# Kernel optimization log

Hardware: AMD Instinct MI355X
Metric: run time of the kernel (lower is better)

## Reference

```python
import jax, jax.numpy as jnp
import numpy as np

D_MODEL = 768
MLP_DIM = 3072
N_EXPERTS = 8
TOP_K = 2
GROUP_DET = 1024
GROUP_CLS = 128


def _route(x, wr, k, capacity):
    """Deterministic top-k softmax router with capacity (vmoe-style).

    x: [G, S, d], wr: [d, E]. Returns dispatch [G,S,E,C] (0/1) and
    combine [G,S,E,C] (gate-weighted).
    """
    G, S, _ = x.shape
    E = wr.shape[1]
    gates = jax.nn.softmax(jnp.einsum('gsd,de->gse', x, wr))  # [G,S,E]
    gval, gidx = jax.lax.top_k(gates, k)                      # [G,S,k]
    # rank-major ordering: all rank-0 choices first, then rank-1, ...
    idx = jnp.swapaxes(gidx, 1, 2).reshape(G, k * S)          # [G,kS]
    val = jnp.swapaxes(gval, 1, 2).reshape(G, k * S)
    oh = jax.nn.one_hot(idx, E, dtype=x.dtype)                # [G,kS,E]
    # position of each assignment in its expert's buffer
    pos = jnp.take_along_axis(jnp.cumsum(oh, axis=1), idx[..., None], axis=2)[..., 0] - 1.0
    keep = (pos < capacity).astype(x.dtype)                   # drop overflow tokens
    posc = jnp.where(pos < capacity, pos, 0.0).astype(jnp.int32)
    slot = jax.nn.one_hot(posc, capacity, dtype=x.dtype)      # [G,kS,C]
    disp = oh[:, :, :, None] * slot[:, :, None, :] * keep[:, :, None, None]  # [G,kS,E,C]
    disp = disp.reshape(G, k, S, E, capacity)
    combine = (disp * val.reshape(G, k, S, 1, 1)).sum(axis=1)  # [G,S,E,C]
    dispatch = disp.sum(axis=1)                                # [G,S,E,C]
    return dispatch, combine


def _expert_mlp(xe, w1, b1, w2, b2):
    # xe: [E,G,C,d]; per-expert params w1:[E,d,m], b1:[E,m], w2:[E,m,d], b2:[E,d]
    h = jax.nn.gelu(jnp.einsum('egcd,edm->egcm', xe, w1) + b1[:, None, None, :])
    return jnp.einsum('egcm,emd->egcd', h, w2) + b2[:, None, None, :]


def _moe_stream(x3, group_size, wr, w1, b1, w2, b2):
    B, S, d = x3.shape
    x = x3.reshape(-1, group_size, d)                         # [G,gs,d]
    capacity = group_size * TOP_K // N_EXPERTS
    dispatch, combine = _route(x, wr, TOP_K, capacity)
    xe = jnp.einsum('gsec,gsd->egcd', dispatch, x)            # gather to experts
    ye = _expert_mlp(xe, w1, b1, w2, b2)                      # grouped MLP
    y = jnp.einsum('gsec,egcd->gsd', combine, ye)             # weighted scatter back
    return y.reshape(B, S, d)


def setup_inputs() -> dict:
    key = jax.random.key(0)
    ks = jax.random.split(key, 8)
    xav1 = float(np.sqrt(6.0 / (D_MODEL + MLP_DIM)))
    xavr = float(np.sqrt(6.0 / (D_MODEL + N_EXPERTS)))
    return {
        'inputs_det': jax.random.normal(ks[0], (8, 1024, D_MODEL), jnp.float32),
        'inputs_cls': jax.random.normal(ks[1], (8, 128, D_MODEL), jnp.float32),
        'wr_det': jax.random.uniform(ks[2], (D_MODEL, N_EXPERTS), jnp.float32, -xavr, xavr),
        'wr_cls': jax.random.uniform(ks[3], (D_MODEL, N_EXPERTS), jnp.float32, -xavr, xavr),
        'w1': jax.random.uniform(ks[4], (N_EXPERTS, D_MODEL, MLP_DIM), jnp.float32, -xav1, xav1),
        'b1': jax.random.normal(ks[5], (N_EXPERTS, MLP_DIM), jnp.float32) * 1e-6,
        'w2': jax.random.uniform(ks[6], (N_EXPERTS, MLP_DIM, D_MODEL), jnp.float32, -xav1, xav1),
        'b2': jax.random.normal(ks[7], (N_EXPERTS, D_MODEL), jnp.float32) * 1e-6,
    }


def reference(inputs_det, inputs_cls, wr_det, wr_cls, w1, b1, w2, b2):
    out_det = _moe_stream(inputs_det, GROUP_DET, wr_det, w1, b1, w2, b2)
    out_cls = _moe_stream(inputs_cls, GROUP_CLS, wr_cls, w1, b1, w2, b2)
    return (out_det, out_cls)
```

## Files before the change

### kernel.cpp

```cpp
#include <hip/hip_runtime.h>
#include <hip/hip_bf16.h>
#include <math.h>

typedef __bf16 bf16;
typedef __bf16 bf16x8 __attribute__((ext_vector_type(8)));
typedef __bf16 bf16x4 __attribute__((ext_vector_type(4)));
typedef float  f32x4  __attribute__((ext_vector_type(4)));

#define D_MODEL 768
#define MLP_DIM 3072

#define SZ_W1T   ((size_t)8*3072*768*2)
#define SZ_W2T   ((size_t)8*768*3072*2)
#define SZ_XED   ((size_t)8*8*256*768*2)
#define SZ_XEC   ((size_t)8*8*32*768*2)
#define SZ_HD    ((size_t)8*2048*3072*2)
#define SZ_HC    ((size_t)8*256*3072*2)
#define SZ_YED   ((size_t)8*2048*768*2)
#define SZ_YEC   ((size_t)8*256*768*2)
#define SZ_RID   ((size_t)8192*8)
#define SZ_RGD   ((size_t)8192*8)
#define SZ_RIC   ((size_t)1024*8)
#define SZ_RGC   ((size_t)1024*8)
#define SZ_STD   ((size_t)8*8*256*4)
#define SZ_STC   ((size_t)8*8*32*4)
#define SZ_TSD   ((size_t)2*8192*4)
#define SZ_TSC   ((size_t)2*1024*4)

#define OFF_W1T  ((size_t)0)
#define OFF_W2T  (OFF_W1T + SZ_W1T)
#define OFF_XED  (OFF_W2T + SZ_W2T)
#define OFF_XEC  (OFF_XED + SZ_XED)
#define OFF_HD   (OFF_XEC + SZ_XEC)
#define OFF_HC   (OFF_HD  + SZ_HD)
#define OFF_YED  (OFF_HC  + SZ_HC)
#define OFF_YEC  (OFF_YED + SZ_YED)
#define OFF_RID  (OFF_YEC + SZ_YEC)
#define OFF_RGD  (OFF_RID + SZ_RID)
#define OFF_RIC  (OFF_RGD + SZ_RGD)
#define OFF_RGC  (OFF_RIC + SZ_RIC)
#define OFF_STD  (OFF_RGC + SZ_RGC)
#define OFF_STC  (OFF_STD + SZ_STD)
#define OFF_TSD  (OFF_STC + SZ_STC)
#define OFF_TSC  (OFF_TSD + SZ_TSD)

__device__ __forceinline__ void lds_load16(const void* g, void* l) {
  __builtin_amdgcn_global_load_lds((__attribute__((address_space(1))) void*)g,
                                   (__attribute__((address_space(3))) void*)l,
                                   16, 0, 0);
}

__device__ __forceinline__ float gelu_fast(float x) {
  float y = 0.7978845608028654f * x * (1.f + 0.044715f * x * x);
  float e = __expf(2.f * y);
  float t = 1.f - 2.f / (e + 1.f);
  return 0.5f * x * (1.f + t);
}

__global__ void router_kernel(const float* __restrict__ xd, const float* __restrict__ wrd,
                              const float* __restrict__ xc, const float* __restrict__ wrc,
                              int2* __restrict__ rid, float2* __restrict__ rgd,
                              int2* __restrict__ ric, float2* __restrict__ rgc,
                              int splitd) {
  int bid = blockIdx.x;
  const float *x, *wr; int2* ridx; float2* rgate;
  if (bid < splitd) { x = xd; wr = wrd; ridx = rid; rgate = rgd; }
  else { bid -= splitd; x = xc; wr = wrc; ridx = ric; rgate = rgc; }
  int wave = threadIdx.x >> 6;
  int lane = threadIdx.x & 63;
  int t = bid * 4 + wave;
  const float* xr = x + (size_t)t * D_MODEL;
  float acc[8];
#pragma unroll
  for (int e = 0; e < 8; ++e) acc[e] = 0.f;
  for (int d = lane; d < D_MODEL; d += 64) {
    float xv = xr[d];
    const float* w = wr + d * 8;
    float4 a = *(const float4*)w;
    float4 b = *(const float4*)(w + 4);
    acc[0] += xv * a.x; acc[1] += xv * a.y; acc[2] += xv * a.z; acc[3] += xv * a.w;
    acc[4] += xv * b.x; acc[5] += xv * b.y; acc[6] += xv * b.z; acc[7] += xv * b.w;
  }
#pragma unroll
  for (int off = 32; off > 0; off >>= 1) {
#pragma unroll
    for (int e = 0; e < 8; ++e) acc[e] += __shfl_xor(acc[e], off, 64);
  }
  float mx = acc[0];
#pragma unroll
  for (int e = 1; e < 8; ++e) mx = fmaxf(mx, acc[e]);
  float p[8]; float z = 0.f;
#pragma unroll
  for (int e = 0; e < 8; ++e) { p[e] = __expf(acc[e] - mx); z += p[e]; }
  int i1 = 0;
#pragma unroll
  for (int e = 1; e < 8; ++e) if (p[e] > p[i1]) i1 = e;
  int i2 = (i1 == 0) ? 1 : 0;
#pragma unroll
  for (int e = 0; e < 8; ++e) if (e != i1 && p[e] > p[i2]) i2 = e;
  if (lane == 0) {
    float inv = 1.f / z;
    ridx[t]  = make_int2(i1, i2);
    rgate[t] = make_float2(p[i1] * inv, p[i2] * inv);
  }
}

__global__ void positions_kernel(const int2* __restrict__ rid, int* __restrict__ std_,
                                 int* __restrict__ tsd_, const int2* __restrict__ ric,
                                 int* __restrict__ stc_, int* __restrict__ tsc_) {
  __shared__ int2 sh[1024];
  int bid = blockIdx.x;
  const int2* ridx; int *slot_token, *tok_slot; int S, C, g;
  if (bid < 8) { ridx = rid; slot_token = std_; tok_slot = tsd_; S = 1024; C = 256; g = bid; }
  else { ridx = ric; slot_token = stc_; tok_slot = tsc_; S = 128; C = 32; g = bid - 8; }
  int lane = threadIdx.x;
  int ntok = 8 * S;
  for (int i = lane; i < S; i += 64) sh[i] = ridx[g * S + i];
  __builtin_amdgcn_s_waitcnt(0);
  unsigned long long ltmask = (1ull << lane) - 1ull;
  int cnt[8];
#pragma unroll
  for (int e = 0; e < 8; ++e) cnt[e] = 0;
  int nch = (2 * S) >> 6;
  for (int ch = 0; ch < nch; ++ch) {
    int a = (ch << 6) + lane;
    int r = (a >= S) ? 1 : 0;
    int s = a - r * S;
    int2 id = sh[s];
    int  e  = r ? id.y : id.x;
    unsigned long long mymask = 0;
    int add[8];
#pragma unroll
    for (int ee = 0; ee < 8; ++ee) {
      unsigned long long mk = __ballot(e == ee);
      if (e == ee) mymask = mk;
      add[ee] = __popcll(mk);
    }
    int pos = cnt[e] + __popcll(mymask & ltmask);
    int sl = (e * 8 + g) * C + pos;
    if (pos < C) slot_token[sl] = s;
    tok_slot[r * ntok + g * S + s] = (pos < C) ? sl : -1;
#pragma unroll
    for (int ee = 0; ee < 8; ++ee) cnt[ee] += add[ee];
  }
}

__global__ void gather_kernel(const float* __restrict__ xd, const int* __restrict__ std_,
                              bf16* __restrict__ xed, const float* __restrict__ xc,
                              const int* __restrict__ stc_, bf16* __restrict__ xec,
                              int splitd) {
  int bid = blockIdx.x;
  const float* x; const int* slot_token; bf16* xe; int S, C;
  if (bid < splitd) { x = xd; slot_token = std_; xe = xed; S = 1024; C = 256; }
  else { bid -= splitd; x = xc; slot_token = stc_; xe = xec; S = 128; C = 32; }
  int slot = bid * 4 + (threadIdx.x >> 6);
  int lane = threadIdx.x & 63;
  int g = (slot / C) & 7;
  int s = slot_token[slot];
  bf16* dst = xe + (size_t)slot * D_MODEL;
  const float* xr = x + ((size_t)g * S + (s < 0 ? 0 : s)) * D_MODEL;
#pragma unroll
  for (int j = 0; j < 3; ++j) {
    int idx = j * 256 + lane * 4;
    float4 v;
    if (s >= 0) v = *(const float4*)(xr + idx);
    else        v = make_float4(0.f, 0.f, 0.f, 0.f);
    bf16 o[4] = {(bf16)v.x, (bf16)v.y, (bf16)v.z, (bf16)v.w};
    *(uint2*)(dst + idx) = *(const uint2*)o;
  }
}

__global__ void convt_kernel(const float* __restrict__ w1, bf16* __restrict__ w1t,
                             const float* __restrict__ w2, bf16* __restrict__ w2t) {
  __shared__ float tile[32][33];
  int bid = blockIdx.x;
  const float* src; bf16* dst; int K, N;
  if (bid < 18432) { src = w1; dst = w1t; K = 768; N = 3072; }
  else { bid -= 18432; src = w2; dst = w2t; K = 3072; N = 768; }
  int e = bid / 2304;
  int t = bid - e * 2304;
  int tiles_x = N >> 5;
  int ky = t / tiles_x;
  int n0 = (t - ky * tiles_x) * 32, k0 = ky * 32;
  const float* S_ = src + (size_t)e * K * N;
  bf16* D_ = dst + (size_t)e * K * N;
  int tx = threadIdx.x & 31, ty = threadIdx.x >> 5;
#pragma unroll
  for (int i = 0; i < 4; ++i)
    tile[ty + 8 * i][tx] = S_[(size_t)(k0 + ty + 8 * i) * N + (n0 + tx)];
  __syncthreads();
  int tid = threadIdx.x;
  int n = tid >> 3, kc = (tid & 7) * 4;
  bf16 o[4] = {(bf16)tile[kc][n], (bf16)tile[kc + 1][n], (bf16)tile[kc + 2][n], (bf16)tile[kc + 3][n]};
  *(uint2*)(D_ + (size_t)(n0 + n) * K + (k0 + kc)) = *(const uint2*)o;
}

__global__ void combine_kernel(const int* __restrict__ tsd_, const float2* __restrict__ rgd,
                               const bf16* __restrict__ yed, float* __restrict__ outd,
                               const int* __restrict__ tsc_, const float2* __restrict__ rgc,
                               const bf16* __restrict__ yec, float* __restrict__ outc,
                               int splitd) {
  int bid = blockIdx.x;
  const int* tok_slot; const float2* rgate; const bf16* ye; float* out; int ntok;
  if (bid < splitd) { tok_slot = tsd_; rgate = rgd; ye = yed; out = outd; ntok = 8192; }
  else { bid -= splitd; tok_slot = tsc_; rgate = rgc; ye = yec; out = outc; ntok = 1024; }
  int t = bid * 4 + (threadIdx.x >> 6);
  int lane = threadIdx.x & 63;
  int s1 = tok_slot[t];
  int s2 = tok_slot[ntok + t];
  float2 gg = rgate[t];
  float g1 = (s1 < 0) ? 0.f : gg.x;
  float g2 = (s2 < 0) ? 0.f : gg.y;
  const bf16* y1 = ye + (size_t)(s1 < 0 ? 0 : s1) * D_MODEL;
  const bf16* y2 = ye + (size_t)(s2 < 0 ? 0 : s2) * D_MODEL;
  float* orow = out + (size_t)t * D_MODEL;
#pragma unroll
  for (int j = 0; j < 3; ++j) {
    int idx = j * 256 + lane * 4;
    bf16x4 a = *(const bf16x4*)(y1 + idx);
    bf16x4 b = *(const bf16x4*)(y2 + idx);
    float4 o;
    o.x = g1 * (float)a[0] + g2 * (float)b[0];
    o.y = g1 * (float)a[1] + g2 * (float)b[1];
    o.z = g1 * (float)a[2] + g2 * (float)b[2];
    o.w = g1 * (float)a[3] + g2 * (float)b[3];
    *(float4*)(orow + idx) = o;
  }
}

template <int GELU>
__launch_bounds__(256, 3)
__global__ void gemm_mfma(const bf16* __restrict__ Adet, const bf16* __restrict__ Acls,
                          const bf16* __restrict__ Btall, const float* __restrict__ biasall,
                          int Mdet, int Mcls, int N, int K,
                          int Nmd, int Nmc, int Nn, int minner, int splitd,
                          bf16* __restrict__ Odet, bf16* __restrict__ Ocls) {
  int bid = blockIdx.x;
  const bf16* Aall; bf16* Oall; int M, Nm;
  if (bid < splitd) { Aall = Adet; Oall = Odet; M = Mdet; Nm = Nmd; }
  else { bid -= splitd; Aall = Acls; Oall = Ocls; M = Mcls; Nm = Nmc; }
  const int e   = bid & 7;
  const int seq = bid >> 3;
  int m_t, n_t;
  if (minner) { n_t = seq / Nm; m_t = seq - n_t * Nm; }
  else        { m_t = seq / Nn; n_t = seq - m_t * Nn; }
  const int n0 = n_t * 128;
  const int m0 = m_t * 128;
  const int tid  = threadIdx.x;
  const int wave = tid >> 6, lane = tid & 63;
  const int wm = (wave >> 1) * 64, wn = (wave & 1) * 64;
  const int lrow = lane & 15, lquad = lane >> 4;

  __shared__ __align__(16) bf16 smem[16384];
  bf16* As = smem;
  bf16* Bs = smem + 8192;

  const bf16* A  = Aall  + (size_t)e * M * K;
  const bf16* Bt = Btall + (size_t)e * N * K;

  const int srow = tid >> 3;
  const int gq   = (tid & 7) ^ (srow & 7);
  const bf16* Asrc = A  + (size_t)(m0 + srow) * K + gq * 8;
  const bf16* Bsrc = Bt + (size_t)(n0 + srow) * K + gq * 8;
  char* AsB = (char*)As;
  char* BsB = (char*)Bs;
  const int ldsw = wave * 1024;

  const float* bias = biasall + (size_t)e * N;
  float bfr[4];
#pragma unroll
  for (int ni = 0; ni < 4; ++ni) bfr[ni] = bias[n0 + wn + ni * 16 + lrow];

  f32x4 acc[4][4];
#pragma unroll
  for (int mi = 0; mi < 4; ++mi)
#pragma unroll
    for (int ni = 0; ni < 4; ++ni) acc[mi][ni] = {0.f, 0.f, 0.f, 0.f};

  const int xsw = lrow & 7;
  const int nsteps = K >> 6;
  for (int kt = 0; kt < nsteps; ++kt) {
    const bf16* a0 = Asrc + kt * 64;
    const bf16* b0 = Bsrc + kt * 64;
#pragma unroll
    for (int rd = 0; rd < 4; ++rd) {
      lds_load16(a0 + (size_t)(rd * 32) * K, AsB + rd * 4096 + ldsw);
      lds_load16(b0 + (size_t)(rd * 32) * K, BsB + rd * 4096 + ldsw);
    }
    __syncthreads();
#pragma unroll
    for (int h = 0; h < 2; ++h) {
      bf16x8 fa[4], fb[4];
      const int ca = ((h * 4 + lquad) ^ xsw) * 8;
#pragma unroll
      for (int i = 0; i < 4; ++i) {
        fa[i] = *(const bf16x8*)(As + (wm + i * 16 + lrow) * 64 + ca);
        fb[i] = *(const bf16x8*)(Bs + (wn + i * 16 + lrow) * 64 + ca);
      }
#pragma unroll
      for (int mi = 0; mi < 4; ++mi)
#pragma unroll
        for (int ni = 0; ni < 4; ++ni)
          acc[mi][ni] = __builtin_amdgcn_mfma_f32_16x16x32_bf16(fa[mi], fb[ni], acc[mi][ni], 0, 0, 0);
    }
    __syncthreads();
  }

#pragma unroll
  for (int mi = 0; mi < 4; ++mi) {
#pragma unroll
    for (int r = 0; r < 4; ++r) {
      int row = wm + mi * 16 + lquad * 4 + r;
#pragma unroll
      for (int ni = 0; ni < 4; ++ni) {
        int colL = wn + ni * 16 + lrow;
        float v = acc[mi][ni][r] + bfr[ni];
        if (GELU) v = gelu_fast(v);
        int chunk = (colL >> 3) ^ (row & 7);
        smem[row * 128 + chunk * 8 + (colL & 7)] = (bf16)v;
      }
    }
  }
  __syncthreads();
  bf16* O = Oall + (size_t)e * M * N;
#pragma unroll
  for (int it = 0; it < 8; ++it) {
    int idx = it * 256 + tid;
    int row = idx >> 4;
    int ck  = idx & 15;
    int pchunk = ck ^ (row & 7);
    bf16x8 vv = *(const bf16x8*)(smem + row * 128 + pchunk * 8);
    *(bf16x8*)(O + (size_t)(m0 + row) * N + n0 + ck * 8) = vv;
  }
}

extern "C" void kernel_launch(void* const* d_in, const int* in_sizes, int n_in,
                              void* d_out, int out_size, void* d_ws, size_t ws_size,
                              hipStream_t stream) {
  (void)in_sizes; (void)n_in; (void)ws_size; (void)out_size;
  const float* x_det  = (const float*)d_in[0];
  const float* x_cls  = (const float*)d_in[1];
  const float* wr_det = (const float*)d_in[2];
  const float* wr_cls = (const float*)d_in[3];
  const float* w1     = (const float*)d_in[4];
  const float* b1     = (const float*)d_in[5];
  const float* w2     = (const float*)d_in[6];
  const float* b2     = (const float*)d_in[7];
  float* out = (float*)d_out;
  char*  ws  = (char*)d_ws;

  bf16*   w1t    = (bf16*)(ws + OFF_W1T);
  bf16*   w2t    = (bf16*)(ws + OFF_W2T);
  bf16*   xe_det = (bf16*)(ws + OFF_XED);
  bf16*   xe_cls = (bf16*)(ws + OFF_XEC);
  bf16*   h_det  = (bf16*)(ws + OFF_HD);
  bf16*   h_cls  = (bf16*)(ws + OFF_HC);
  bf16*   ye_det = (bf16*)(ws + OFF_YED);
  bf16*   ye_cls = (bf16*)(ws + OFF_YEC);
  int2*   ri_det = (int2*)(ws + OFF_RID);
  float2* rg_det = (float2*)(ws + OFF_RGD);
  int2*   ri_cls = (int2*)(ws + OFF_RIC);
  float2* rg_cls = (float2*)(ws + OFF_RGC);
  int*    st_det = (int*)(ws + OFF_STD);
  int*    st_cls = (int*)(ws + OFF_STC);
  int*    ts_det = (int*)(ws + OFF_TSD);
  int*    ts_cls = (int*)(ws + OFF_TSC);

  hipMemsetAsync(ws + OFF_STD, 0xFF, SZ_STD + SZ_STC, stream);

  convt_kernel<<<2 * 18432, 256, 0, stream>>>(w1, w1t, w2, w2t);

  router_kernel<<<2048 + 256, 256, 0, stream>>>(x_det, wr_det, x_cls, wr_cls,
                                                ri_det, rg_det, ri_cls, rg_cls, 2048);
  positions_kernel<<<16, 64, 0, stream>>>(ri_det, st_det, ts_det, ri_cls, st_cls, ts_cls);

  gather_kernel<<<4096 + 512, 256, 0, stream>>>(x_det, st_det, xe_det, x_cls, st_cls, xe_cls, 4096);

  gemm_mfma<1><<<8 * 16 * 24 + 8 * 2 * 24, 256, 0, stream>>>(
      xe_det, xe_cls, w1t, b1, 2048, 256, 3072, 768,
      16, 2, 24, 1, 8 * 16 * 24, h_det, h_cls);

  gemm_mfma<0><<<8 * 16 * 6 + 8 * 2 * 6, 256, 0, stream>>>(
      h_det, h_cls, w2t, b2, 2048, 256, 768, 3072,
      16, 2, 6, 0, 8 * 16 * 6, ye_det, ye_cls);

  combine_kernel<<<2048 + 256, 256, 0, stream>>>(ts_det, rg_det, ye_det, out,
                                                 ts_cls, rg_cls, ye_cls,
                                                 out + (size_t)8192 * 768, 2048);
}
```

Before: 483.7 us.

## Fuse router into weight conversion, drop memset, template GEMM K, cheaper GELU

The router and weight-transpose/bf16-conversion kernels are merged into one launch, and the separate memset of slot tables is replaced by having positions_kernel fill unused slots with -1. The GEMM takes K as a compile-time template parameter, with its k-loop unrolled fully for the first GEMM and by four for the second. GELU is rewritten as x*sigmoid form using a fast reciprocal and a clamped exponent. Together these aim to cut launch overhead and loop/ALU cost, at the price of larger code and a slightly different GELU approximation.

Result: slower. 498.7 us (+3.1%).

```diff
diff --git a/kernel.cpp b/kernel.cpp
--- a/kernel.cpp
+++ b/kernel.cpp
@@ -51,129 +51,65 @@
 }
 
 __device__ __forceinline__ float gelu_fast(float x) {
-  float y = 0.7978845608028654f * x * (1.f + 0.044715f * x * x);
-  float e = __expf(2.f * y);
-  float t = 1.f - 2.f / (e + 1.f);
-  return 0.5f * x * (1.f + t);
-}
-
-__global__ void router_kernel(const float* __restrict__ xd, const float* __restrict__ wrd,
-                              const float* __restrict__ xc, const float* __restrict__ wrc,
-                              int2* __restrict__ rid, float2* __restrict__ rgd,
-                              int2* __restrict__ ric, float2* __restrict__ rgc,
-                              int splitd) {
-  int bid = blockIdx.x;
-  const float *x, *wr; int2* ridx; float2* rgate;
-  if (bid < splitd) { x = xd; wr = wrd; ridx = rid; rgate = rgd; }
-  else { bid -= splitd; x = xc; wr = wrc; ridx = ric; rgate = rgc; }
-  int wave = threadIdx.x >> 6;
-  int lane = threadIdx.x & 63;
-  int t = bid * 4 + wave;
-  const float* xr = x + (size_t)t * D_MODEL;
-  float acc[8];
-#pragma unroll
-  for (int e = 0; e < 8; ++e) acc[e] = 0.f;
-  for (int d = lane; d < D_MODEL; d += 64) {
-    float xv = xr[d];
-    const float* w = wr + d * 8;
-    float4 a = *(const float4*)w;
-    float4 b = *(const float4*)(w + 4);
-    acc[0] += xv * a.x; acc[1] += xv * a.y; acc[2] += xv * a.z; acc[3] += xv * a.w;
-    acc[4] += xv * b.x; acc[5] += xv * b.y; acc[6] += xv * b.z; acc[7] += xv * b.w;
-  }
-#pragma unroll
-  for (int off = 32; off > 0; off >>= 1) {
-#pragma unroll
-    for (int e = 0; e < 8; ++e) acc[e] += __shfl_xor(acc[e], off, 64);
-  }
-  float mx = acc[0];
-#pragma unroll
-  for (int e = 1; e < 8; ++e) mx = fmaxf(mx, acc[e]);
-  float p[8]; float z = 0.f;
-#pragma unroll
-  for (int e = 0; e < 8; ++e) { p[e] = __expf(acc[e] - mx); z += p[e]; }
-  int i1 = 0;
-#pragma unroll
-  for (int e = 1; e < 8; ++e) if (p[e] > p[i1]) i1 = e;
-  int i2 = (i1 == 0) ? 1 : 0;
-#pragma unroll
-  for (int e = 0; e < 8; ++e) if (e != i1 && p[e] > p[i2]) i2 = e;
-  if (lane == 0) {
-    float inv = 1.f / z;
-    ridx[t]  = make_int2(i1, i2);
-    rgate[t] = make_float2(p[i1] * inv, p[i2] * inv);
-  }
-}
-
-__global__ void positions_kernel(const int2* __restrict__ rid, int* __restrict__ std_,
-                                 int* __restrict__ tsd_, const int2* __restrict__ ric,
-                                 int* __restrict__ stc_, int* __restrict__ tsc_) {
-  __shared__ int2 sh[1024];
-  int bid = blockIdx.x;
-  const int2* ridx; int *slot_token, *tok_slot; int S, C, g;
-  if (bid < 8) { ridx = rid; slot_token = std_; tok_slot = tsd_; S = 1024; C = 256; g = bid; }
-  else { ridx = ric; slot_token = stc_; tok_slot = tsc_; S = 128; C = 32; g = bid - 8; }
-  int lane = threadIdx.x;
-  int ntok = 8 * S;
-  for (int i = lane; i < S; i += 64) sh[i] = ridx[g * S + i];
-  __builtin_amdgcn_s_waitcnt(0);
-  unsigned long long ltmask = (1ull << lane) - 1ull;
-  int cnt[8];
-#pragma unroll
-  for (int e = 0; e < 8; ++e) cnt[e] = 0;
-  int nch = (2 * S) >> 6;
-  for (int ch = 0; ch < nch; ++ch) {
-    int a = (ch << 6) + lane;
-    int r = (a >= S) ? 1 : 0;
-    int s = a - r * S;
-    int2 id = sh[s];
-    int  e  = r ? id.y : id.x;
-    unsigned long long mymask = 0;
-    int add[8];
-#pragma unroll
-    for (int ee = 0; ee < 8; ++ee) {
-      unsigned long long mk = __ballot(e == ee);
-      if (e == ee) mymask = mk;
-      add[ee] = __popcll(mk);
-    }
-    int pos = cnt[e] + __popcll(mymask & ltmask);
-    int sl = (e * 8 + g) * C + pos;
-    if (pos < C) slot_token[sl] = s;
-    tok_slot[r * ntok + g * S + s] = (pos < C) ? sl : -1;
-#pragma unroll
-    for (int ee = 0; ee < 8; ++ee) cnt[ee] += add[ee];
-  }
-}
-
-__global__ void gather_kernel(const float* __restrict__ xd, const int* __restrict__ std_,
-                              bf16* __restrict__ xed, const float* __restrict__ xc,
-                              const int* __restrict__ stc_, bf16* __restrict__ xec,
-                              int splitd) {
-  int bid = blockIdx.x;
-  const float* x; const int* slot_token; bf16* xe; int S, C;
-  if (bid < splitd) { x = xd; slot_token = std_; xe = xed; S = 1024; C = 256; }
-  else { bid -= splitd; x = xc; slot_token = stc_; xe = xec; S = 128; C = 32; }
-  int slot = bid * 4 + (threadIdx.x >> 6);
-  int lane = threadIdx.x & 63;
-  int g = (slot / C) & 7;
-  int s = slot_token[slot];
-  bf16* dst = xe + (size_t)slot * D_MODEL;
-  const float* xr = x + ((size_t)g * S + (s < 0 ? 0 : s)) * D_MODEL;
-#pragma unroll
-  for (int j = 0; j < 3; ++j) {
-    int idx = j * 256 + lane * 4;
-    float4 v;
-    if (s >= 0) v = *(const float4*)(xr + idx);
-    else        v = make_float4(0.f, 0.f, 0.f, 0.f);
-    bf16 o[4] = {(bf16)v.x, (bf16)v.y, (bf16)v.z, (bf16)v.w};
-    *(uint2*)(dst + idx) = *(const uint2*)o;
-  }
-}
-
-__global__ void convt_kernel(const float* __restrict__ w1, bf16* __restrict__ w1t,
-                             const float* __restrict__ w2, bf16* __restrict__ w2t) {
+  float x2 = x * x;
+  float z = x * __builtin_fmaf(-0.07135481627f, x2, -1.5957691216f);
+  z = fminf(z, 80.f);
+  float e = __expf(z);
+  return x * __builtin_amdgcn_rcpf(1.f + e);
+}
+
+__global__ void convt_router_kernel(const float* __restrict__ w1, bf16* __restrict__ w1t,
+                                    const float* __restrict__ w2, bf16* __restrict__ w2t,
+                                    const float* __restrict__ xd, const float* __restrict__ wrd,
+                                    const float* __restrict__ xc, const float* __restrict__ wrc,
+                                    int2* __restrict__ rid, float2* __restrict__ rgd,
+                                    int2* __restrict__ ric, float2* __restrict__ rgc) {
+  int bid = blockIdx.x;
+  if (bid < 2304) {
+    const float *x, *wr; int2* ridx; float2* rgate;
+    if (bid < 2048) { x = xd; wr = wrd; ridx = rid; rgate = rgd; }
+    else { bid -= 2048; x = xc; wr = wrc; ridx = ric; rgate = rgc; }
+    int wave = threadIdx.x >> 6;
+    int lane = threadIdx.x & 63;
+    int t = bid * 4 + wave;
+    const float* xr = x + (size_t)t * D_MODEL;
+    float acc[8];
+#pragma unroll
+    for (int e = 0; e < 8; ++e) acc[e] = 0.f;
+    for (int d = lane; d < D_MODEL; d += 64) {
+      float xv = xr[d];
+      const float* w = wr + d * 8;
+      float4 a = *(const float4*)w;
+      float4 b = *(const float4*)(w + 4);
+      acc[0] += xv * a.x; acc[1] += xv * a.y; acc[2] += xv * a.z; acc[3] += xv * a.w;
+      acc[4] += xv * b.x; acc[5] += xv * b.y; acc[6] += xv * b.z; acc[7] += xv * b.w;
+    }
+#pragma unroll
+    for (int off = 32; off > 0; off >>= 1) {
+#pragma unroll
+      for (int e = 0; e < 8; ++e) acc[e] += __shfl_xor(acc[e], off, 64);
+    }
+    float mx = acc[0];
+#pragma unroll
+    for (int e = 1; e < 8; ++e) mx = fmaxf(mx, acc[e]);
+    float p[8]; float z = 0.f;
+#pragma unroll
+    for (int e = 0; e < 8; ++e) { p[e] = __expf(acc[e] - mx); z += p[e]; }
+    int i1 = 0;
+#pragma unroll
+    for (int e = 1; e < 8; ++e) if (p[e] > p[i1]) i1 = e;
+    int i2 = (i1 == 0) ? 1 : 0;
+#pragma unroll
+    for (int e = 0; e < 8; ++e) if (e != i1 && p[e] > p[i2]) i2 = e;
+    if (lane == 0) {
+      float inv = 1.f / z;
+      ridx[t]  = make_int2(i1, i2);
+      rgate[t] = make_float2(p[i1] * inv, p[i2] * inv);
+    }
+    return;
+  }
+  bid -= 2304;
   __shared__ float tile[32][33];
-  int bid = blockIdx.x;
   const float* src; bf16* dst; int K, N;
   if (bid < 18432) { src = w1; dst = w1t; K = 768; N = 3072; }
   else { bid -= 18432; src = w2; dst = w2t; K = 3072; N = 768; }
@@ -193,6 +129,76 @@
   int n = tid >> 3, kc = (tid & 7) * 4;
   bf16 o[4] = {(bf16)tile[kc][n], (bf16)tile[kc + 1][n], (bf16)tile[kc + 2][n], (bf16)tile[kc + 3][n]};
   *(uint2*)(D_ + (size_t)(n0 + n) * K + (k0 + kc)) = *(const uint2*)o;
+}
+
+__global__ void positions_kernel(const int2* __restrict__ rid, int* __restrict__ std_,
+                                 int* __restrict__ tsd_, const int2* __restrict__ ric,
+                                 int* __restrict__ stc_, int* __restrict__ tsc_) {
+  __shared__ int2 sh[1024];
+  int bid = blockIdx.x;
+  const int2* ridx; int *slot_token, *tok_slot; int S, C, g;
+  if (bid < 8) { ridx = rid; slot_token = std_; tok_slot = tsd_; S = 1024; C = 256; g = bid; }
+  else { ridx = ric; slot_token = stc_; tok_slot = tsc_; S = 128; C = 32; g = bid - 8; }
+  int lane = threadIdx.x;
+  int ntok = 8 * S;
+  for (int i = lane; i < S; i += 64) sh[i] = ridx[g * S + i];
+  __builtin_amdgcn_s_waitcnt(0);
+  unsigned long long ltmask = (1ull << lane) - 1ull;
+  int cnt[8];
+#pragma unroll
+  for (int e = 0; e < 8; ++e) cnt[e] = 0;
+  int nch = (2 * S) >> 6;
+  for (int ch = 0; ch < nch; ++ch) {
+    int a = (ch << 6) + lane;
+    int r = (a >= S) ? 1 : 0;
+    int s = a - r * S;
+    int2 id = sh[s];
+    int  e  = r ? id.y : id.x;
+    unsigned long long mymask = 0;
+    int add[8];
+#pragma unroll
+    for (int ee = 0; ee < 8; ++ee) {
+      unsigned long long mk = __ballot(e == ee);
+      if (e == ee) mymask = mk;
+      add[ee] = __popcll(mk);
+    }
+    int pos = cnt[e] + __popcll(mymask & ltmask);
+    int sl = (e * 8 + g) * C + pos;
+    if (pos < C) slot_token[sl] = s;
+    tok_slot[r * ntok + g * S + s] = (pos < C) ? sl : -1;
+#pragma unroll
+    for (int ee = 0; ee < 8; ++ee) cnt[ee] += add[ee];
+  }
+#pragma unroll
+  for (int e = 0; e < 8; ++e) {
+    for (int i = cnt[e] + lane; i < C; i += 64)
+      slot_token[(e * 8 + g) * C + i] = -1;
+  }
+}
+
+__global__ void gather_kernel(const float* __restrict__ xd, const int* __restrict__ std_,
+                              bf16* __restrict__ xed, const float* __restrict__ xc,
+                              const int* __restrict__ stc_, bf16* __restrict__ xec,
+                              int splitd) {
+  int bid = blockIdx.x;
+  const float* x; const int* slot_token; bf16* xe; int S, C;
+  if (bid < splitd) { x = xd; slot_token = std_; xe = xed; S = 1024; C = 256; }
+  else { bid -= splitd; x = xc; slot_token = stc_; xe = xec; S = 128; C = 32; }
+  int slot = bid * 4 + (threadIdx.x >> 6);
+  int lane = threadIdx.x & 63;
+  int g = (slot / C) & 7;
+  int s = slot_token[slot];
+  bf16* dst = xe + (size_t)slot * D_MODEL;
+  const float* xr = x + ((size_t)g * S + (s < 0 ? 0 : s)) * D_MODEL;
+#pragma unroll
+  for (int j = 0; j < 3; ++j) {
+    int idx = j * 256 + lane * 4;
+    float4 v;
+    if (s >= 0) v = *(const float4*)(xr + idx);
+    else        v = make_float4(0.f, 0.f, 0.f, 0.f);
+    bf16 o[4] = {(bf16)v.x, (bf16)v.y, (bf16)v.z, (bf16)v.w};
+    *(uint2*)(dst + idx) = *(const uint2*)o;
+  }
 }
 
 __global__ void combine_kernel(const int* __restrict__ tsd_, const float2* __restrict__ rgd,
@@ -228,13 +234,14 @@
   }
 }
 
-template <int GELU>
+template <int GELU, int KT>
 __launch_bounds__(256, 3)
 __global__ void gemm_mfma(const bf16* __restrict__ Adet, const bf16* __restrict__ Acls,
                           const bf16* __restrict__ Btall, const float* __restrict__ biasall,
-                          int Mdet, int Mcls, int N, int K,
+                          int Mdet, int Mcls, int N,
                           int Nmd, int Nmc, int Nn, int minner, int splitd,
                           bf16* __restrict__ Odet, bf16* __restrict__ Ocls) {
+  constexpr int K = KT * 64;
   int bid = blockIdx.x;
   const bf16* Aall; bf16* Oall; int M, Nm;
   if (bid < splitd) { Aall = Adet; Oall = Odet; M = Mdet; Nm = Nmd; }
@@ -278,32 +285,36 @@
     for (int ni = 0; ni < 4; ++ni) acc[mi][ni] = {0.f, 0.f, 0.f, 0.f};
 
   const int xsw = lrow & 7;
-  const int nsteps = K >> 6;
-  for (int kt = 0; kt < nsteps; ++kt) {
-    const bf16* a0 = Asrc + kt * 64;
-    const bf16* b0 = Bsrc + kt * 64;
-#pragma unroll
-    for (int rd = 0; rd < 4; ++rd) {
-      lds_load16(a0 + (size_t)(rd * 32) * K, AsB + rd * 4096 + ldsw);
-      lds_load16(b0 + (size_t)(rd * 32) * K, BsB + rd * 4096 + ldsw);
-    }
-    __syncthreads();
-#pragma unroll
-    for (int h = 0; h < 2; ++h) {
-      bf16x8 fa[4], fb[4];
-      const int ca = ((h * 4 + lquad) ^ xsw) * 8;
-#pragma unroll
-      for (int i = 0; i < 4; ++i) {
-        fa[i] = *(const bf16x8*)(As + (wm + i * 16 + lrow) * 64 + ca);
-        fb[i] = *(const bf16x8*)(Bs + (wn + i * 16 + lrow) * 64 + ca);
+  constexpr int UNR = (KT <= 16) ? KT : 4;
+  for (int kt0 = 0; kt0 < KT; kt0 += UNR) {
+#pragma unroll
+    for (int u = 0; u < UNR; ++u) {
+      const int kt = kt0 + u;
+      const bf16* a0 = Asrc + kt * 64;
+      const bf16* b0 = Bsrc + kt * 64;
+#pragma unroll
+      for (int rd = 0; rd < 4; ++rd) {
+        lds_load16(a0 + (size_t)(rd * 32) * K, AsB + rd * 4096 + ldsw);
+        lds_load16(b0 + (size_t)(rd * 32) * K, BsB + rd * 4096 + ldsw);
       }
-#pragma unroll
-      for (int mi = 0; mi < 4; ++mi)
-#pragma unroll
-        for (int ni = 0; ni < 4; ++ni)
-          acc[mi][ni] = __builtin_amdgcn_mfma_f32_16x16x32_bf16(fa[mi], fb[ni], acc[mi][ni], 0, 0, 0);
-    }
-    __syncthreads();
+      __syncthreads();
+#pragma unroll
+      for (int h = 0; h < 2; ++h) {
+        bf16x8 fa[4], fb[4];
+        const int ca = ((h * 4 + lquad) ^ xsw) * 8;
+#pragma unroll
+        for (int i = 0; i < 4; ++i) {
+          fa[i] = *(const bf16x8*)(As + (wm + i * 16 + lrow) * 64 + ca);
+          fb[i] = *(const bf16x8*)(Bs + (wn + i * 16 + lrow) * 64 + ca);
+        }
+#pragma unroll
+        for (int mi = 0; mi < 4; ++mi)
+#pragma unroll
+          for (int ni = 0; ni < 4; ++ni)
+            acc[mi][ni] = __builtin_amdgcn_mfma_f32_16x16x32_bf16(fa[mi], fb[ni], acc[mi][ni], 0, 0, 0);
+      }
+      __syncthreads();
+    }
   }
 
 #pragma unroll
@@ -366,22 +377,20 @@
   int*    ts_det = (int*)(ws + OFF_TSD);
   int*    ts_cls = (int*)(ws + OFF_TSC);
 
-  hipMemsetAsync(ws + OFF_STD, 0xFF, SZ_STD + SZ_STC, stream);
-
-  convt_kernel<<<2 * 18432, 256, 0, stream>>>(w1, w1t, w2, w2t);
-
-  router_kernel<<<2048 + 256, 256, 0, stream>>>(x_det, wr_det, x_cls, wr_cls,
-                                                ri_det, rg_det, ri_cls, rg_cls, 2048);
+  convt_router_kernel<<<2304 + 2 * 18432, 256, 0, stream>>>(
+      w1, w1t, w2, w2t, x_det, wr_det, x_cls, wr_cls,
+      ri_det, rg_det, ri_cls, rg_cls);
+
   positions_kernel<<<16, 64, 0, stream>>>(ri_det, st_det, ts_det, ri_cls, st_cls, ts_cls);
 
   gather_kernel<<<4096 + 512, 256, 0, stream>>>(x_det, st_det, xe_det, x_cls, st_cls, xe_cls, 4096);
 
-  gemm_mfma<1><<<8 * 16 * 24 + 8 * 2 * 24, 256, 0, stream>>>(
-      xe_det, xe_cls, w1t, b1, 2048, 256, 3072, 768,
+  gemm_mfma<1, 12><<<8 * 16 * 24 + 8 * 2 * 24, 256, 0, stream>>>(
+      xe_det, xe_cls, w1t, b1, 2048, 256, 3072,
       16, 2, 24, 1, 8 * 16 * 24, h_det, h_cls);
 
-  gemm_mfma<0><<<8 * 16 * 6 + 8 * 2 * 6, 256, 0, stream>>>(
-      h_det, h_cls, w2t, b2, 2048, 256, 768, 3072,
+  gemm_mfma<0, 48><<<8 * 16 * 6 + 8 * 2 * 6, 256, 0, stream>>>(
+      h_det, h_cls, w2t, b2, 2048, 256, 768,
       16, 2, 6, 0, 8 * 16 * 6, ye_det, ye_cls);
 
   combine_kernel<<<2048 + 256, 256, 0, stream>>>(ts_det, rg_det, ye_det, out,
```
